# Optimization experiments

Hardware: AMD Instinct MI355X
Metric: run time of the kernel (lower is better)

## Reference

```python
import jax, jax.numpy as jnp
import numpy as np

MARGIN = 1.0  # init kwarg
BIG = 1e9     # finite sentinel for masked reductions (dist in [0, 2])


def setup_inputs() -> dict:
    key = jax.random.key(0)
    k1, k2 = jax.random.split(key)
    embeddings = jax.random.normal(k1, (8192, 256), dtype=jnp.float32)
    labels = jax.random.randint(k2, (8192,), 0, 128)
    return {"embeddings": embeddings, "labels": labels}


def reference(embeddings, labels):
    # cosine distance matrix: 1 - x_hat @ x_hat^T, clamped at 0
    norm = jnp.linalg.norm(embeddings, axis=1, keepdims=True)
    x = embeddings / jnp.maximum(norm, 1e-12)  # matches F.normalize eps
    dist = jnp.clip(1.0 - x @ x.T, 0.0, None)  # (B, B)

    same = labels[:, None] == labels[None, :]
    eye = jnp.eye(labels.shape[0], dtype=bool)
    pos_mask = same & ~eye   # same label, different index
    neg_mask = ~same         # different label

    # hard mining: hardest positive (max dist), hardest negative (min dist)
    pos_dist = jnp.max(jnp.where(pos_mask, dist, -BIG), axis=1)  # (B,)
    neg_dist = jnp.min(jnp.where(neg_mask, dist, BIG), axis=1)   # (B,)

    valid = pos_mask.any(axis=1) & neg_mask.any(axis=1)          # (B,)
    per_anchor = jnp.maximum(pos_dist - neg_dist + MARGIN, 0.0)
    loss_sum = jnp.sum(jnp.where(valid, per_anchor, 0.0))
    count = jnp.sum(valid).astype(dist.dtype)
    return jnp.where(count > 0, loss_sum / jnp.maximum(count, 1.0), 0.0)
```

## Files before the change

### kernel.cpp

```cpp
#include <hip/hip_runtime.h>
#include <hip/hip_bf16.h>


constexpr int NB = 8192;
constexpr int ND = 256;
constexpr int BI = 256;
constexpr int BJ = 64;
constexpr int JSPLIT = 16;
constexpr int JRANGE = NB / JSPLIT;
constexpr int NITER = JRANGE / BJ;

typedef __attribute__((ext_vector_type(8))) short bf16x8;
typedef __attribute__((ext_vector_type(4))) float f32x4;

typedef __attribute__((address_space(3))) unsigned int lds_u32;
typedef __attribute__((address_space(1))) const unsigned int g_u32;

__device__ inline void load_lds16(const unsigned short* g, unsigned short* l) {
    __builtin_amdgcn_global_load_lds((g_u32*)g, (lds_u32*)l, 16, 0, 0);
}

__device__ inline unsigned short f2bf(float v) {
    __hip_bfloat16 b = __float2bfloat16(v);
    return *reinterpret_cast<unsigned short*>(&b);
}

__global__ __launch_bounds__(256) void norm_kernel(const float* __restrict__ X,
                                                   unsigned short* __restrict__ Xbt,
                                                   float* accum, int* done) {
    const int t = threadIdx.x;
    const int rb = blockIdx.x * 32;
    const int r = t >> 3, e = t & 7;
    if (blockIdx.x == 0 && t == 0) { accum[0] = 0.f; accum[1] = 0.f; *done = 0; }

    const float4* src = (const float4*)(X + (size_t)(rb + r) * ND + e * 32);
    float4 v[8];
    #pragma unroll
    for (int k = 0; k < 8; k++) v[k] = src[k];

    float s = 0.f;
    #pragma unroll
    for (int k = 0; k < 8; k++) {
        s += v[k].x * v[k].x; s += v[k].y * v[k].y;
        s += v[k].z * v[k].z; s += v[k].w * v[k].w;
    }
    #pragma unroll
    for (int m = 1; m <= 4; m <<= 1) s += __shfl_xor(s, m, 64);
    const float sc = 1.0f / fmaxf(sqrtf(s), 1e-12f);

    #pragma unroll
    for (int k = 0; k < 4; k++) {
        const float* f = (const float*)&v[2 * k];
        unsigned short tmp[8];
        #pragma unroll
        for (int q = 0; q < 8; q++) tmp[q] = f2bf(f[q] * sc);
        *(bf16x8*)(Xbt + ((size_t)(e * 4 + k) * NB + rb + r) * 8) = *(bf16x8*)tmp;
    }
}

__global__ __launch_bounds__(512, 4) void mine_kernel(
    const unsigned short* __restrict__ Xbt, const int* __restrict__ labels,
    float* __restrict__ posP, float* __restrict__ negP) {
    __shared__ __align__(16) unsigned short Bt[2][32 * 512];
    __shared__ float Lall[JRANGE];

    const int tid = threadIdx.x;
    const int w = tid >> 6;
    const int lane = tid & 63;
    const int quad = lane >> 4;
    const int l16 = lane & 15;

    const int rowbase = blockIdx.x * BI + w * 32;
    const int jstart = blockIdx.y * JRANGE;

    Lall[tid] = (float)labels[jstart + tid];

    bf16x8 afrag[2][8];
    #pragma unroll
    for (int rs = 0; rs < 2; rs++)
        #pragma unroll
        for (int kc = 0; kc < 8; kc++) {
            const size_t u = (size_t)(kc * 4 + quad) * NB + (rowbase + rs * 16 + l16);
            afrag[rs][kc] = *(const bf16x8*)(Xbt + u * 8);
        }

    float flr[2][4];
    float minK[2][4], maxK[2][4];
    #pragma unroll
    for (int rs = 0; rs < 2; rs++)
        #pragma unroll
        for (int r = 0; r < 4; r++) {
            flr[rs][r] = (float)labels[rowbase + rs * 16 + quad * 4 + r];
            minK[rs][r] = 1e30f;
            maxK[rs][r] = -1e30f;
        }

    auto stage = [&](int buf, int jt) {
        const int jbase = jstart + jt * BJ;
        #pragma unroll
        for (int s = 0; s < 4; s++) {
            const int rg = w * 4 + s;
            const int kc = rg >> 2, nfi = rg & 3;
            const size_t u = (size_t)(kc * 4 + quad) * NB + (jbase + nfi * 16 + l16);
            load_lds16(Xbt + u * 8, &Bt[buf][rg * 512]);
        }
    };

    stage(0, 0);
    __syncthreads();

    for (int jt = 0; jt < NITER; jt++) {
        const int cur = jt & 1;
        if (jt + 1 < NITER) stage(cur ^ 1, jt + 1);

        #pragma unroll
        for (int nf = 0; nf < 4; nf++) {
            const float flc = Lall[jt * BJ + nf * 16 + l16];
            f32x4 acc[2];
            #pragma unroll
            for (int rs = 0; rs < 2; rs++) acc[rs] = (f32x4){0.f, 0.f, 0.f, 0.f};
            #pragma unroll
            for (int kc = 0; kc < 8; kc++) {
                const bf16x8 b = *(const bf16x8*)(&Bt[cur][(kc * 4 + nf) * 512 + lane * 8]);
                #pragma unroll
                for (int rs = 0; rs < 2; rs++)
                    acc[rs] = __builtin_amdgcn_mfma_f32_16x16x32_bf16(
                        afrag[rs][kc], b, acc[rs], 0, 0, 0);
            }
            #pragma unroll
            for (int rs = 0; rs < 2; rs++)
                #pragma unroll
                for (int r = 0; r < 4; r++) {
                    const float d = flr[rs][r] - flc;
                    const float uu = fminf(fabsf(d), 1.0f);
                    const float key = fmaf(uu, 8.0f, acc[rs][r]);
                    minK[rs][r] = fminf(minK[rs][r], key);
                    maxK[rs][r] = fmaxf(maxK[rs][r], key);
                }
        }
        __syncthreads();
    }

    #pragma unroll
    for (int rs = 0; rs < 2; rs++)
        #pragma unroll
        for (int r = 0; r < 4; r++) {
            float p = minK[rs][r], n = maxK[rs][r];
            #pragma unroll
            for (int m = 1; m <= 8; m <<= 1) {
                p = fminf(p, __shfl_xor(p, m, 64));
                n = fmaxf(n, __shfl_xor(n, m, 64));
            }
            if (l16 == 0) {
                const int row = rowbase + rs * 16 + quad * 4 + r;
                posP[blockIdx.y * NB + row] = p;
                negP[blockIdx.y * NB + row] = n;
            }
        }
}

__global__ __launch_bounds__(256) void finish_kernel(
    const float* __restrict__ posP, const float* __restrict__ negP,
    float* accum, int* done, float* __restrict__ out) {
    const int i = blockIdx.x * 256 + threadIdx.x;
    float p = 1e30f, n = -1e30f;
    #pragma unroll
    for (int s = 0; s < JSPLIT; s++) {
        p = fminf(p, posP[s * NB + i]);
        n = fmaxf(n, negP[s * NB + i]);
    }
    const bool valid = (p < 4.0f) && (n > 4.0f);
    const float pos_d = fmaxf(1.0f - p, 0.0f);
    const float neg_d = fmaxf(1.0f - (n - 8.0f), 0.0f);
    float per = valid ? fmaxf(pos_d - neg_d + 1.0f, 0.0f) : 0.0f;
    float cnt = valid ? 1.0f : 0.0f;
    #pragma unroll
    for (int off = 32; off > 0; off >>= 1) {
        per += __shfl_down(per, off, 64);
        cnt += __shfl_down(cnt, off, 64);
    }
    __shared__ float sp[4], sc[4];
    const int wv = threadIdx.x >> 6, ln = threadIdx.x & 63;
    if (ln == 0) { sp[wv] = per; sc[wv] = cnt; }
    __syncthreads();
    if (threadIdx.x == 0) {
        atomicAdd(&accum[0], sp[0] + sp[1] + sp[2] + sp[3]);
        atomicAdd(&accum[1], sc[0] + sc[1] + sc[2] + sc[3]);
        __threadfence();
        const int old = atomicAdd(done, 1);
        if (old == (int)gridDim.x - 1) {
            const float s = __hip_atomic_load(&accum[0], __ATOMIC_RELAXED,
                                              __HIP_MEMORY_SCOPE_AGENT);
            const float c = __hip_atomic_load(&accum[1], __ATOMIC_RELAXED,
                                              __HIP_MEMORY_SCOPE_AGENT);
            out[0] = (c > 0.f) ? s / fmaxf(c, 1.f) : 0.f;
        }
    }
}

extern "C" void kernel_launch(void* const* d_in, const int* in_sizes, int n_in,
                              void* d_out, int out_size, void* d_ws, size_t ws_size,
                              hipStream_t stream) {
    const float* X = (const float*)d_in[0];
    const int* labels = (const int*)d_in[1];
    float* out = (float*)d_out;

    char* ws = (char*)d_ws;
    unsigned short* Xbt = (unsigned short*)ws;
    float* posP = (float*)(ws + (size_t)4 * 1024 * 1024);
    float* negP = posP + JSPLIT * NB;
    float* accum = negP + JSPLIT * NB;
    int* done = (int*)(accum + 2);

    norm_kernel<<<NB / 32, 256, 0, stream>>>(X, Xbt, accum, done);
    mine_kernel<<<dim3(NB / BI, JSPLIT), 512, 0, stream>>>(
        (const unsigned short*)Xbt, labels, posP, negP);
    finish_kernel<<<NB / 256, 256, 0, stream>>>(posP, negP, accum, done, out);
}
```

Before: 98.21 us.

## Exploit distance-matrix symmetry with triangular tiles and atomic row/column reductions

The mining kernel now launches only the upper-triangular 256x256 tile pairs of the symmetric distance matrix. Each tile reduces its min/max keys both along rows, as before, and along columns, through LDS and a cross-wave reduction. Partial results go to per-anchor order-preserving uint keys via atomicMin/atomicMax, replacing the JSPLIT partial arrays and the multi-way merge in the finish kernel. This roughly halves the MFMA work. In exchange it adds column-reduction shuffles, extra barriers and global atomics, and drops the LDS double buffering, so tile loads no longer overlap with compute.

```diff
diff --git a/kernel.cpp b/kernel.cpp
--- a/kernel.cpp
+++ b/kernel.cpp
@@ -4,11 +4,11 @@
 
 constexpr int NB = 8192;
 constexpr int ND = 256;
-constexpr int BI = 256;
+constexpr int TI = 256;
 constexpr int BJ = 64;
-constexpr int JSPLIT = 16;
-constexpr int JRANGE = NB / JSPLIT;
-constexpr int NITER = JRANGE / BJ;
+constexpr int NT = NB / TI;
+constexpr int NPAIR = NT * (NT + 1) / 2;
+constexpr int NITER = TI / BJ;
 
 typedef __attribute__((ext_vector_type(8))) short bf16x8;
 typedef __attribute__((ext_vector_type(4))) float f32x4;
@@ -25,13 +25,26 @@
     return *reinterpret_cast<unsigned short*>(&b);
 }
 
+__device__ inline unsigned int fkey(float f) {
+    unsigned int u = __float_as_uint(f);
+    return (u & 0x80000000u) ? ~u : (u | 0x80000000u);
+}
+__device__ inline float funkey(unsigned int m) {
+    unsigned int u = (m & 0x80000000u) ? (m ^ 0x80000000u) : ~m;
+    return __uint_as_float(u);
+}
+
 __global__ __launch_bounds__(256) void norm_kernel(const float* __restrict__ X,
                                                    unsigned short* __restrict__ Xbt,
+                                                   unsigned int* __restrict__ posM,
+                                                   unsigned int* __restrict__ negM,
                                                    float* accum, int* done) {
     const int t = threadIdx.x;
     const int rb = blockIdx.x * 32;
     const int r = t >> 3, e = t & 7;
-    if (blockIdx.x == 0 && t == 0) { accum[0] = 0.f; accum[1] = 0.f; *done = 0; }
+    const int g = blockIdx.x * 256 + t;
+    if (g < NB) { posM[g] = 0xFFFFFFFFu; negM[g] = 0u; }
+    if (g == 0) { accum[0] = 0.f; accum[1] = 0.f; *done = 0; }
 
     const float4* src = (const float4*)(X + (size_t)(rb + r) * ND + e * 32);
     float4 v[8];
@@ -60,9 +73,10 @@
 
 __global__ __launch_bounds__(512, 4) void mine_kernel(
     const unsigned short* __restrict__ Xbt, const int* __restrict__ labels,
-    float* __restrict__ posP, float* __restrict__ negP) {
-    __shared__ __align__(16) unsigned short Bt[2][32 * 512];
-    __shared__ float Lall[JRANGE];
+    unsigned int* __restrict__ posM, unsigned int* __restrict__ negM) {
+    __shared__ __align__(16) unsigned short Bt[32 * 512];
+    __shared__ float Lall[TI];
+    __shared__ float colMn[8][BJ], colMx[8][BJ];
 
     const int tid = threadIdx.x;
     const int w = tid >> 6;
@@ -70,10 +84,14 @@
     const int quad = lane >> 4;
     const int l16 = lane & 15;
 
-    const int rowbase = blockIdx.x * BI + w * 32;
-    const int jstart = blockIdx.y * JRANGE;
-
-    Lall[tid] = (float)labels[jstart + tid];
+    int ti = 0, rem = blockIdx.x;
+    while (rem >= NT - ti) { rem -= NT - ti; ti++; }
+    const int tj = ti + rem;
+
+    const int rowbase = ti * TI + w * 32;
+    const int jstart = tj * TI;
+
+    if (tid < TI) Lall[tid] = (float)labels[jstart + tid];
 
     bf16x8 afrag[2][8];
     #pragma unroll
@@ -95,24 +113,21 @@
             maxK[rs][r] = -1e30f;
         }
 
-    auto stage = [&](int buf, int jt) {
+    auto stage = [&](int jt) {
         const int jbase = jstart + jt * BJ;
         #pragma unroll
         for (int s = 0; s < 4; s++) {
             const int rg = w * 4 + s;
             const int kc = rg >> 2, nfi = rg & 3;
             const size_t u = (size_t)(kc * 4 + quad) * NB + (jbase + nfi * 16 + l16);
-            load_lds16(Xbt + u * 8, &Bt[buf][rg * 512]);
+            load_lds16(Xbt + u * 8, Bt + rg * 512);
         }
     };
 
-    stage(0, 0);
+    stage(0);
     __syncthreads();
 
     for (int jt = 0; jt < NITER; jt++) {
-        const int cur = jt & 1;
-        if (jt + 1 < NITER) stage(cur ^ 1, jt + 1);
-
         #pragma unroll
         for (int nf = 0; nf < 4; nf++) {
             const float flc = Lall[jt * BJ + nf * 16 + l16];
@@ -121,12 +136,13 @@
             for (int rs = 0; rs < 2; rs++) acc[rs] = (f32x4){0.f, 0.f, 0.f, 0.f};
             #pragma unroll
             for (int kc = 0; kc < 8; kc++) {
-                const bf16x8 b = *(const bf16x8*)(&Bt[cur][(kc * 4 + nf) * 512 + lane * 8]);
+                const bf16x8 b = *(const bf16x8*)(Bt + (kc * 4 + nf) * 512 + lane * 8);
                 #pragma unroll
                 for (int rs = 0; rs < 2; rs++)
                     acc[rs] = __builtin_amdgcn_mfma_f32_16x16x32_bf16(
                         afrag[rs][kc], b, acc[rs], 0, 0, 0);
             }
+            float cP = 1e30f, cN = -1e30f;
             #pragma unroll
             for (int rs = 0; rs < 2; rs++)
                 #pragma unroll
@@ -136,7 +152,31 @@
                     const float key = fmaf(uu, 8.0f, acc[rs][r]);
                     minK[rs][r] = fminf(minK[rs][r], key);
                     maxK[rs][r] = fmaxf(maxK[rs][r], key);
+                    cP = fminf(cP, key);
+                    cN = fmaxf(cN, key);
                 }
+            cP = fminf(cP, __shfl_xor(cP, 16, 64));
+            cP = fminf(cP, __shfl_xor(cP, 32, 64));
+            cN = fmaxf(cN, __shfl_xor(cN, 16, 64));
+            cN = fmaxf(cN, __shfl_xor(cN, 32, 64));
+            if (quad == 0) {
+                colMn[w][nf * 16 + l16] = cP;
+                colMx[w][nf * 16 + l16] = cN;
+            }
+        }
+        __syncthreads();
+        if (jt + 1 < NITER) stage(jt + 1);
+        if (tid < BJ) {
+            float m = colMn[0][tid];
+            #pragma unroll
+            for (int ww = 1; ww < 8; ww++) m = fminf(m, colMn[ww][tid]);
+            atomicMin(&posM[jstart + jt * BJ + tid], fkey(m));
+        } else if (tid < 2 * BJ) {
+            const int c = tid - BJ;
+            float M = colMx[0][c];
+            #pragma unroll
+            for (int ww = 1; ww < 8; ww++) M = fmaxf(M, colMx[ww][c]);
+            atomicMax(&negM[jstart + jt * BJ + c], fkey(M));
         }
         __syncthreads();
     }
@@ -153,22 +193,18 @@
             }
             if (l16 == 0) {
                 const int row = rowbase + rs * 16 + quad * 4 + r;
-                posP[blockIdx.y * NB + row] = p;
-                negP[blockIdx.y * NB + row] = n;
+                atomicMin(&posM[row], fkey(p));
+                atomicMax(&negM[row], fkey(n));
             }
         }
 }
 
 __global__ __launch_bounds__(256) void finish_kernel(
-    const float* __restrict__ posP, const float* __restrict__ negP,
+    const unsigned int* __restrict__ posM, const unsigned int* __restrict__ negM,
     float* accum, int* done, float* __restrict__ out) {
     const int i = blockIdx.x * 256 + threadIdx.x;
-    float p = 1e30f, n = -1e30f;
-    #pragma unroll
-    for (int s = 0; s < JSPLIT; s++) {
-        p = fminf(p, posP[s * NB + i]);
-        n = fmaxf(n, negP[s * NB + i]);
-    }
+    const float p = funkey(posM[i]);
+    const float n = funkey(negM[i]);
     const bool valid = (p < 4.0f) && (n > 4.0f);
     const float pos_d = fmaxf(1.0f - p, 0.0f);
     const float neg_d = fmaxf(1.0f - (n - 8.0f), 0.0f);
@@ -207,13 +243,13 @@
 
     char* ws = (char*)d_ws;
     unsigned short* Xbt = (unsigned short*)ws;
-    float* posP = (float*)(ws + (size_t)4 * 1024 * 1024);
-    float* negP = posP + JSPLIT * NB;
-    float* accum = negP + JSPLIT * NB;
+    unsigned int* posM = (unsigned int*)(ws + (size_t)4 * 1024 * 1024);
+    unsigned int* negM = posM + NB;
+    float* accum = (float*)(negM + NB);
     int* done = (int*)(accum + 2);
 
-    norm_kernel<<<NB / 32, 256, 0, stream>>>(X, Xbt, accum, done);
-    mine_kernel<<<dim3(NB / BI, JSPLIT), 512, 0, stream>>>(
-        (const unsigned short*)Xbt, labels, posP, negP);
-    finish_kernel<<<NB / 256, 256, 0, stream>>>(posP, negP, accum, done, out);
-}
+    norm_kernel<<<NB / 32, 256, 0, stream>>>(X, Xbt, posM, negM, accum, done);
+    mine_kernel<<<NPAIR, 512, 0, stream>>>(
+        (const unsigned short*)Xbt, labels, posM, negM);
+    finish_kernel<<<NB / 256, 256, 0, stream>>>(posM, negM, accum, done, out);
+}
```

Result: slower. 111.2 us (+13.2%).
